# Kernel tuning notes

Measured on AMD Instinct MI355X. Metric: run time of the kernel, lower is better.

Reference implementation:

```python
import jax, jax.numpy as jnp
import numpy as np

B, C_IN, C_OUT, K, IN_SIZE = 16, 32, 32, 16, 8192
OUT_SIZE = IN_SIZE - K  # 8176


def setup_inputs() -> dict:
    key = jax.random.key(0)
    kx, kw, kb = jax.random.split(key, 3)
    x = jax.random.normal(kx, (B, C_IN, IN_SIZE), dtype=jnp.float32)
    # locally-connected (non-weight-shared) conv weights generated by cppn at init
    w = jax.random.normal(kw, (C_OUT, C_IN, OUT_SIZE, K), dtype=jnp.float32)
    b = jax.random.normal(kb, (C_OUT,), dtype=jnp.float32)
    return {"x": x, "w": w, "b": b}


def reference(x, w, b):
    # sliding-window gather: idxs[o, t] = o + t, shape (O, K)
    idxs = jnp.arange(OUT_SIZE)[:, None] + jnp.arange(K)[None, :]
    windows = x[:, :, idxs]  # (B, C_in, O, K)
    # per-output-position weights: contract over C_in and K only
    out = jnp.einsum("bcok,dcok->bdo", windows, w)  # (B, C_out, O)
    return jax.nn.relu(out + b[None, :, None])
```

## Files before the change

### kernel.cpp

```cpp
#include <hip/hip_runtime.h>
#include <cstddef>

constexpr int Bn  = 16;
constexpr int CIc = 32;
constexpr int COc = 32;
constexpr int Kc  = 16;
constexpr int IN  = 8192;
constexpr int OUTL = 8176;

constexpr int O_B  = 16;
constexpr int CCH  = 8;
constexpr int NPOS = 32;
constexpr int BST  = 20;
constexpr int NCHUNK = CIc / CCH;

__global__ __launch_bounds__(256, 3)
void conv1d_cppn_kernel(const float* __restrict__ x, const float* __restrict__ w,
                        const float* __restrict__ bias, float* __restrict__ out) {
    __shared__ float xs[2][CCH][NPOS][BST];

    const int tid = threadIdx.x;
    const int og = tid & 15;
    const int dg = tid >> 4;
    const int o0 = blockIdx.x * O_B;
    const int o  = o0 + og;
    const int dbase = dg * 2;

    const int sp4 = tid & 7;
    const int sb  = (tid >> 3) & 15;
    const int cl0 = tid >> 7;

    float acc[2][16];
#pragma unroll
    for (int i = 0; i < 2; ++i)
#pragma unroll
        for (int j = 0; j < 16; ++j) acc[i][j] = 0.f;

#pragma unroll
    for (int q = 0; q < 4; ++q) {
        const int cl = cl0 + 2 * q;
        const float4 v = *reinterpret_cast<const float4*>(
            &x[((size_t)sb * CIc + cl) * IN + o0 + sp4 * 4]);
        float (*prow)[BST] = &xs[0][cl][sp4 * 4];
        prow[0][sb] = v.x; prow[1][sb] = v.y; prow[2][sb] = v.z; prow[3][sb] = v.w;
    }
    __syncthreads();

    int buf = 0;
    for (int chunk = 0; chunk < NCHUNK; ++chunk) {
        float4 xr[4];
        if (chunk + 1 < NCHUNK) {
            const int c0n = (chunk + 1) * CCH;
#pragma unroll
            for (int q = 0; q < 4; ++q) {
                xr[q] = *reinterpret_cast<const float4*>(
                    &x[((size_t)sb * CIc + c0n + cl0 + 2 * q) * IN + o0 + sp4 * 4]);
            }
        }

        const int c0 = chunk * CCH;
#pragma unroll 2
        for (int cc = 0; cc < CCH; ++cc) {
            const int c = c0 + cc;
            float wreg[2][16];
#pragma unroll
            for (int jd = 0; jd < 2; ++jd) {
                const float4* wp = reinterpret_cast<const float4*>(
                    w + (((size_t)(dbase + jd) * CIc + c) * OUTL + o) * Kc);
#pragma unroll
                for (int q = 0; q < 4; ++q) {
                    const float4 v = wp[q];
                    wreg[jd][q * 4 + 0] = v.x;
                    wreg[jd][q * 4 + 1] = v.y;
                    wreg[jd][q * 4 + 2] = v.z;
                    wreg[jd][q * 4 + 3] = v.w;
                }
            }
#pragma unroll
            for (int k = 0; k < Kc; ++k) {
                const float* xrow = &xs[buf][cc][og + k][0];
                float xv[16];
                *reinterpret_cast<float4*>(&xv[0])  = *reinterpret_cast<const float4*>(xrow);
                *reinterpret_cast<float4*>(&xv[4])  = *reinterpret_cast<const float4*>(xrow + 4);
                *reinterpret_cast<float4*>(&xv[8])  = *reinterpret_cast<const float4*>(xrow + 8);
                *reinterpret_cast<float4*>(&xv[12]) = *reinterpret_cast<const float4*>(xrow + 12);
#pragma unroll
                for (int jd = 0; jd < 2; ++jd) {
                    const float wk = wreg[jd][k];
#pragma unroll
                    for (int jb = 0; jb < 16; ++jb) {
                        acc[jd][jb] += wk * xv[jb];
                    }
                }
            }
        }

        if (chunk + 1 < NCHUNK) {
#pragma unroll
            for (int q = 0; q < 4; ++q) {
                const int cl = cl0 + 2 * q;
                float (*prow)[BST] = &xs[buf ^ 1][cl][sp4 * 4];
                prow[0][sb] = xr[q].x; prow[1][sb] = xr[q].y;
                prow[2][sb] = xr[q].z; prow[3][sb] = xr[q].w;
            }
            __syncthreads();
        }
        buf ^= 1;
    }

#pragma unroll
    for (int jd = 0; jd < 2; ++jd) {
        const float bv = bias[dbase + jd];
#pragma unroll
        for (int jb = 0; jb < 16; ++jb) {
            float v = acc[jd][jb] + bv;
            out[((size_t)jb * COc + (dbase + jd)) * OUTL + o] = v > 0.f ? v : 0.f;
        }
    }
}

extern "C" void kernel_launch(void* const* d_in, const int* in_sizes, int n_in,
                              void* d_out, int out_size, void* d_ws, size_t ws_size,
                              hipStream_t stream) {
    const float* x    = (const float*)d_in[0];
    const float* w    = (const float*)d_in[1];
    const float* bias = (const float*)d_in[2];
    float* out        = (float*)d_out;

    dim3 grid(OUTL / O_B);
    dim3 block(256);
    hipLaunchKernelGGL(conv1d_cppn_kernel, grid, block, 0, stream, x, w, bias, out);
}
```

Measured before the change: 135.7 us.

## Split input channels across thread halves with shared-memory reduction, halve output tile

Each block now covers 8 output positions instead of 16, and its 256 threads split into two groups that each handle half of the input channels. Their partial sums are combined through a shared-memory reduction before bias and ReLU. The goal is twice as many blocks in the grid, which gives more parallelism and latency hiding on the weight stream. In exchange, x staging is no longer double-buffered, an extra reduction with barriers is added, launch bounds drop to 2 blocks per SM, and each block loads a 32-position x window for only 8 outputs, so x traffic per output roughly doubles.

```diff
diff --git a/kernel.cpp b/kernel.cpp
--- a/kernel.cpp
+++ b/kernel.cpp
@@ -8,23 +8,30 @@
 constexpr int IN  = 8192;
 constexpr int OUTL = 8176;
 
-constexpr int O_B  = 16;
+constexpr int O_B  = 8;
 constexpr int CCH  = 8;
 constexpr int NPOS = 32;
 constexpr int BST  = 20;
-constexpr int NCHUNK = CIc / CCH;
 
-__global__ __launch_bounds__(256, 3)
+constexpr int SMEM_FLOATS = 2 * CCH * NPOS * BST;
+
+__global__ __launch_bounds__(256, 2)
 void conv1d_cppn_kernel(const float* __restrict__ x, const float* __restrict__ w,
                         const float* __restrict__ bias, float* __restrict__ out) {
-    __shared__ float xs[2][CCH][NPOS][BST];
+    __shared__ float smem[SMEM_FLOATS];
+    float (*xs)[CCH][NPOS][BST] = reinterpret_cast<float (*)[CCH][NPOS][BST]>(smem);
+    float (*red)[16][O_B][18]   = reinterpret_cast<float (*)[16][O_B][18]>(smem);
 
     const int tid = threadIdx.x;
-    const int og = tid & 15;
-    const int dg = tid >> 4;
+    const int og = tid & 7;
+    const int dg = (tid >> 3) & 15;
+    const int cg = tid >> 7;
     const int o0 = blockIdx.x * O_B;
     const int o  = o0 + og;
     const int dbase = dg * 2;
+
+    const int s0 = (o0 > IN - NPOS) ? (IN - NPOS) : o0;
+    const int d0 = o0 - s0;
 
     const int sp4 = tid & 7;
     const int sb  = (tid >> 3) & 15;
@@ -36,32 +43,21 @@
 #pragma unroll
         for (int j = 0; j < 16; ++j) acc[i][j] = 0.f;
 
+    for (int chunk = 0; chunk < 2; ++chunk) {
+        __syncthreads();
 #pragma unroll
-    for (int q = 0; q < 4; ++q) {
-        const int cl = cl0 + 2 * q;
-        const float4 v = *reinterpret_cast<const float4*>(
-            &x[((size_t)sb * CIc + cl) * IN + o0 + sp4 * 4]);
-        float (*prow)[BST] = &xs[0][cl][sp4 * 4];
-        prow[0][sb] = v.x; prow[1][sb] = v.y; prow[2][sb] = v.z; prow[3][sb] = v.w;
-    }
-    __syncthreads();
+        for (int q = 0; q < 8; ++q) {
+            const int cl = cl0 + 2 * q;
+            const float4 v = *reinterpret_cast<const float4*>(
+                &x[((size_t)sb * CIc + (chunk * 16 + cl)) * IN + s0 + sp4 * 4]);
+            float (*prow)[BST] = &xs[cl >> 3][cl & 7][sp4 * 4];
+            prow[0][sb] = v.x; prow[1][sb] = v.y; prow[2][sb] = v.z; prow[3][sb] = v.w;
+        }
+        __syncthreads();
 
-    int buf = 0;
-    for (int chunk = 0; chunk < NCHUNK; ++chunk) {
-        float4 xr[4];
-        if (chunk + 1 < NCHUNK) {
-            const int c0n = (chunk + 1) * CCH;
-#pragma unroll
-            for (int q = 0; q < 4; ++q) {
-                xr[q] = *reinterpret_cast<const float4*>(
-                    &x[((size_t)sb * CIc + c0n + cl0 + 2 * q) * IN + o0 + sp4 * 4]);
-            }
-        }
-
-        const int c0 = chunk * CCH;
 #pragma unroll 2
         for (int cc = 0; cc < CCH; ++cc) {
-            const int c = c0 + cc;
+            const int c = chunk * 16 + cg * 8 + cc;
             float wreg[2][16];
 #pragma unroll
             for (int jd = 0; jd < 2; ++jd) {
@@ -78,7 +74,7 @@
             }
 #pragma unroll
             for (int k = 0; k < Kc; ++k) {
-                const float* xrow = &xs[buf][cc][og + k][0];
+                const float* xrow = &xs[cg][cc][og + d0 + k][0];
                 float xv[16];
                 *reinterpret_cast<float4*>(&xv[0])  = *reinterpret_cast<const float4*>(xrow);
                 *reinterpret_cast<float4*>(&xv[4])  = *reinterpret_cast<const float4*>(xrow + 4);
@@ -94,27 +90,31 @@
                 }
             }
         }
-
-        if (chunk + 1 < NCHUNK) {
-#pragma unroll
-            for (int q = 0; q < 4; ++q) {
-                const int cl = cl0 + 2 * q;
-                float (*prow)[BST] = &xs[buf ^ 1][cl][sp4 * 4];
-                prow[0][sb] = xr[q].x; prow[1][sb] = xr[q].y;
-                prow[2][sb] = xr[q].z; prow[3][sb] = xr[q].w;
-            }
-            __syncthreads();
-        }
-        buf ^= 1;
     }
 
+    __syncthreads();
+    if (cg == 1) {
 #pragma unroll
-    for (int jd = 0; jd < 2; ++jd) {
-        const float bv = bias[dbase + jd];
+        for (int jd = 0; jd < 2; ++jd) {
+            float* row = &red[jd][dg][og][0];
 #pragma unroll
-        for (int jb = 0; jb < 16; ++jb) {
-            float v = acc[jd][jb] + bv;
-            out[((size_t)jb * COc + (dbase + jd)) * OUTL + o] = v > 0.f ? v : 0.f;
+            for (int s = 0; s < 8; ++s) {
+                *reinterpret_cast<float2*>(row + s * 2) =
+                    make_float2(acc[jd][s * 2], acc[jd][s * 2 + 1]);
+            }
+        }
+    }
+    __syncthreads();
+    if (cg == 0) {
+#pragma unroll
+        for (int jd = 0; jd < 2; ++jd) {
+            const float bv = bias[dbase + jd];
+            const float* row = &red[jd][dg][og][0];
+#pragma unroll
+            for (int jb = 0; jb < 16; ++jb) {
+                float v = acc[jd][jb] + row[jb] + bv;
+                out[((size_t)jb * COc + (dbase + jd)) * OUTL + o] = v > 0.f ? v : 0.f;
+            }
         }
     }
 }
```

Result: slower. 192.8 us (+42.0%).
